# Kernel tuning notes

Measured on AMD Instinct MI355X. Metric: run time of the kernel, lower is better.

## Reference

```python
import jax, jax.numpy as jnp
import numpy as np

N_NODES = 50000
N_EDGES = 400000
IN_DIM = 8
HIDDEN = 768
N_LAYERS = 4
LN_EPS = 1e-5


def setup_inputs() -> dict:
    key = jax.random.key(0)
    ks = jax.random.split(key, 10)
    x = jax.random.normal(ks[0], (N_NODES, IN_DIM), dtype=jnp.float32)
    edge_index = jax.random.randint(ks[1], (2, N_EDGES), 0, N_NODES, dtype=jnp.int32)
    # input projection
    s_in = 1.0 / np.sqrt(IN_DIM)
    Wp = jax.random.uniform(ks[2], (HIDDEN, IN_DIM), jnp.float32, -s_in, s_in)
    bp = jax.random.uniform(ks[3], (HIDDEN,), jnp.float32, -s_in, s_in)
    # stacked per-layer SAGEConv params (all layers have out_c == HIDDEN here)
    s_h = 1.0 / np.sqrt(HIDDEN)
    Wl = jax.random.uniform(ks[4], (N_LAYERS, HIDDEN, HIDDEN), jnp.float32, -s_h, s_h)  # lin_l (aggregated neighbors), has bias
    bl = jax.random.uniform(ks[5], (N_LAYERS, HIDDEN), jnp.float32, -s_h, s_h)
    Wr = jax.random.uniform(ks[6], (N_LAYERS, HIDDEN, HIDDEN), jnp.float32, -s_h, s_h)  # lin_r (root), no bias
    # LayerNorm params
    gamma = jnp.ones((N_LAYERS, HIDDEN), dtype=jnp.float32)
    beta = jnp.zeros((N_LAYERS, HIDDEN), dtype=jnp.float32)
    return {"x": x, "Wp": Wp, "bp": bp, "Wl": Wl, "bl": bl, "Wr": Wr,
            "gamma": gamma, "beta": beta, "edge_index": edge_index}


def _layer_norm(h, g, b):
    mu = jnp.mean(h, axis=-1, keepdims=True)
    var = jnp.mean(jnp.square(h - mu), axis=-1, keepdims=True)
    return (h - mu) * jax.lax.rsqrt(var + LN_EPS) * g + b


def reference(x, Wp, bp, Wl, bl, Wr, gamma, beta, edge_index):
    n = x.shape[0]
    src, dst = edge_index[0], edge_index[1]
    # in-degree per target node, clamped for mean
    deg = jax.ops.segment_sum(jnp.ones_like(dst, dtype=x.dtype), dst, num_segments=n)
    inv_deg = 1.0 / jnp.maximum(deg, 1.0)

    h = x @ Wp.T + bp  # [N, HIDDEN]

    def layer(h, params):
        Wl_i, bl_i, Wr_i, g_i, b_i = params
        # mean aggregation of source features at targets: [N, C]
        agg = jax.ops.segment_sum(h[src], dst, num_segments=n) * inv_deg[:, None]
        out = agg @ Wl_i.T + bl_i + h @ Wr_i.T  # SAGEConv
        out = _layer_norm(jax.nn.silu(out), g_i, b_i)  # norm(silu(conv))
        return out, None

    h, _ = jax.lax.scan(layer, h, (Wl, bl, Wr, gamma, beta))
    return h
```

## Files before the change

### kernel.cpp

```cpp
#include <hip/hip_runtime.h>

#define NN 50000
#define NE 400000
#define HID 768
#define NL 4

typedef short bf16x8_t __attribute__((ext_vector_type(8)));
typedef float f32x4_t __attribute__((ext_vector_type(4)));

__device__ __forceinline__ unsigned short f2bf(float f) {
  union { float f; unsigned int u; } c; c.f = f;
  unsigned int u = c.u;
  u += 0x7FFF + ((u >> 16) & 1);
  return (unsigned short)(u >> 16);
}
__device__ __forceinline__ float bf2f(unsigned short s) {
  union { unsigned int u; float f; } c; c.u = ((unsigned int)s) << 16;
  return c.f;
}

__device__ __forceinline__ void async16(const void* g, void* l) {
  __builtin_amdgcn_global_load_lds((const __attribute__((address_space(1))) void*)g,
                                   (__attribute__((address_space(3))) void*)l,
                                   16, 0, 0);
}

__global__ void k_zero2(int* __restrict__ a, int* __restrict__ b, int n) {
  int i = blockIdx.x * blockDim.x + threadIdx.x;
  if (i < n) { a[i] = 0; b[i] = 0; }
}

__global__ void k_cvt(const float* __restrict__ a, unsigned short* __restrict__ o, int n) {
  int i = blockIdx.x * blockDim.x + threadIdx.x;
  if (i < n) o[i] = f2bf(a[i]);
}

__global__ __launch_bounds__(256) void k_inproj(const float* __restrict__ x,
                                                const float* __restrict__ Wp,
                                                const float* __restrict__ bp,
                                                unsigned short* __restrict__ h) {
  int n = blockIdx.x;
  __shared__ float xs[8];
  if (threadIdx.x < 8) xs[threadIdx.x] = x[n * 8 + threadIdx.x];
  __syncthreads();
  for (int j = threadIdx.x; j < HID; j += 256) {
    const float* w = Wp + j * 8;
    float s = bp[j];
#pragma unroll
    for (int k = 0; k < 8; ++k) s += xs[k] * w[k];
    h[(size_t)n * HID + j] = f2bf(s);
  }
}

__global__ void k_deg(const int* __restrict__ dst, int* __restrict__ deg) {
  int i = blockIdx.x * blockDim.x + threadIdx.x;
  if (i < NE) atomicAdd(&deg[dst[i]], 1);
}

__global__ __launch_bounds__(1024) void k_scan(const int* __restrict__ deg, int* __restrict__ rowptr) {
  __shared__ int sm[1024];
  const int chunk = 49;
  int t = threadIdx.x;
  int start = t * chunk;
  int end = min(start + chunk, NN);
  int local = 0;
  for (int i = start; i < end; ++i) local += deg[i];
  sm[t] = local;
  __syncthreads();
  for (int off = 1; off < 1024; off <<= 1) {
    int v = (t >= off) ? sm[t - off] : 0;
    __syncthreads();
    sm[t] += v;
    __syncthreads();
  }
  int run = sm[t] - local;
  for (int i = start; i < end; ++i) { rowptr[i] = run; run += deg[i]; }
  if (start < NN && end == NN) rowptr[NN] = run;
}

__global__ void k_fill(const int* __restrict__ src, const int* __restrict__ dst,
                       const int* __restrict__ rowptr, int* __restrict__ cursor,
                       int* __restrict__ csr) {
  int i = blockIdx.x * blockDim.x + threadIdx.x;
  if (i < NE) {
    int d = dst[i];
    int pos = atomicAdd(&cursor[d], 1);
    csr[rowptr[d] + pos] = src[i];
  }
}

__global__ __launch_bounds__(192) void k_agg(const unsigned short* __restrict__ h,
                                             const int* __restrict__ csr,
                                             const int* __restrict__ rowptr,
                                             unsigned short* __restrict__ agg) {
  int n = blockIdx.x;
  int t = threadIdx.x;
  int beg = rowptr[n], end = rowptr[n + 1];
  float a0 = 0.f, a1 = 0.f, a2 = 0.f, a3 = 0.f;
  for (int i = beg; i < end; ++i) {
    int s = csr[i];
    ushort4 v = *(const ushort4*)(h + (size_t)s * HID + t * 4);
    a0 += bf2f(v.x); a1 += bf2f(v.y); a2 += bf2f(v.z); a3 += bf2f(v.w);
  }
  float inv = 1.0f / (float)max(end - beg, 1);
  ushort4 o;
  o.x = f2bf(a0 * inv); o.y = f2bf(a1 * inv); o.z = f2bf(a2 * inv); o.w = f2bf(a3 * inv);
  *(ushort4*)(agg + (size_t)n * HID + t * 4) = o;
}

#define BM 224
#define BN 256
#define BKT 32
#define NKT 48
#define NBANDS 224

__global__ __launch_bounds__(512, 2) void k_gemm(const unsigned short* __restrict__ A0,
                                                 const unsigned short* __restrict__ A1,
                                                 const unsigned short* __restrict__ B0,
                                                 const unsigned short* __restrict__ B1,
                                                 const float* __restrict__ bias,
                                                 unsigned short* __restrict__ sact, int M) {
  __shared__ __align__(16) unsigned short As[2][256 * BKT];
  __shared__ __align__(16) unsigned short Bs[2][256 * BKT];

  int b = blockIdx.x;
  int xcd = b & 7;
  int rest = b >> 3;
  int nt3 = rest % 3;
  int g = rest / 3;
  int mband = g * 8 + xcd;
  int m0 = mband * BM;
  int n0 = nt3 * BN;

  int tid = threadIdx.x;
  int lane = tid & 63;
  int w = tid >> 6;
  int wm = w >> 2, wn = w & 3;

  int srow = w * 16 + (lane >> 2);
  int kgg = (lane & 3) ^ ((srow >> 1) & 3);
  size_t aoffg = (size_t)(m0 + srow) * HID + kgg * 8;
  size_t boffg = (size_t)(n0 + srow) * HID + kgg * 8;
  const size_t rstep = (size_t)128 * HID;

  auto stage = [&](int kt, int slot) {
    const unsigned short* A = (kt < 24) ? A0 : A1;
    const unsigned short* B = (kt < 24) ? B0 : B1;
    size_t kk = (size_t)((kt < 24) ? kt : kt - 24) * BKT;
    async16(A + aoffg + kk,         &As[slot][(w * 16) * BKT]);
    async16(B + boffg + kk,         &Bs[slot][(w * 16) * BKT]);
    async16(A + aoffg + rstep + kk, &As[slot][(128 + w * 16) * BKT]);
    async16(B + boffg + rstep + kk, &Bs[slot][(128 + w * 16) * BKT]);
  };

  int mr = lane & 15, kq = lane >> 4;
  int aoff[7], boff[4];
#pragma unroll
  for (int t = 0; t < 7; ++t) {
    int row = wm * 112 + t * 16 + mr;
    aoff[t] = row * BKT + ((kq ^ ((row >> 1) & 3)) * 8);
  }
#pragma unroll
  for (int t = 0; t < 4; ++t) {
    int row = wn * 64 + t * 16 + mr;
    boff[t] = row * BKT + ((kq ^ ((row >> 1) & 3)) * 8);
  }

  f32x4_t acc[7][4] = {};

  stage(0, 0);
  stage(1, 1);

#pragma unroll 2
  for (int T = 0; T < NKT; ++T) {
    int slot = T & 1;
    if (T < NKT - 1) asm volatile("s_waitcnt vmcnt(4)" ::: "memory");
    else             asm volatile("s_waitcnt vmcnt(0)" ::: "memory");
    __builtin_amdgcn_s_barrier();
    asm volatile("" ::: "memory");

    bf16x8_t af[7], bf[4];
#pragma unroll
    for (int t = 0; t < 7; ++t) af[t] = *(const bf16x8_t*)&As[slot][aoff[t]];
#pragma unroll
    for (int t = 0; t < 4; ++t) bf[t] = *(const bf16x8_t*)&Bs[slot][boff[t]];

    __builtin_amdgcn_s_setprio(1);
#pragma unroll
    for (int mt = 0; mt < 7; ++mt)
#pragma unroll
      for (int nt = 0; nt < 4; ++nt)
        acc[mt][nt] = __builtin_amdgcn_mfma_f32_16x16x32_bf16(af[mt], bf[nt], acc[mt][nt], 0, 0, 0);
    __builtin_amdgcn_s_setprio(0);

    asm volatile("s_waitcnt lgkmcnt(0)" ::: "memory");
    __builtin_amdgcn_s_barrier();
    if (T + 2 < NKT) stage(T + 2, slot);
  }

  int col = lane & 15;
  int rq = (lane >> 4) * 4;
#pragma unroll
  for (int mt = 0; mt < 7; ++mt) {
#pragma unroll
    for (int nt = 0; nt < 4; ++nt) {
      int j = n0 + wn * 64 + nt * 16 + col;
      float bv = bias[j];
#pragma unroll
      for (int r = 0; r < 4; ++r) {
        int gm = m0 + wm * 112 + mt * 16 + rq + r;
        if (gm < M) {
          float v = acc[mt][nt][r] + bv;
          float s = v / (1.f + __expf(-v));
          sact[(size_t)gm * HID + j] = f2bf(s);
        }
      }
    }
  }
}

__global__ __launch_bounds__(256) void k_ln(const unsigned short* __restrict__ sact,
                                            const float* __restrict__ gamma,
                                            const float* __restrict__ beta,
                                            unsigned short* __restrict__ hout,
                                            float* __restrict__ fout) {
  int n = blockIdx.x;
  const unsigned short* p = sact + (size_t)n * HID;
  float v[3];
  float sum = 0.f, sq = 0.f;
#pragma unroll
  for (int i = 0; i < 3; ++i) {
    float s = bf2f(p[threadIdx.x + i * 256]);
    v[i] = s; sum += s; sq += s * s;
  }
#pragma unroll
  for (int off = 32; off >= 1; off >>= 1) {
    sum += __shfl_down(sum, off);
    sq  += __shfl_down(sq, off);
  }
  __shared__ float rs[4], rq2[4];
  int wv = threadIdx.x >> 6;
  if ((threadIdx.x & 63) == 0) { rs[wv] = sum; rq2[wv] = sq; }
  __syncthreads();
  if (threadIdx.x == 0) {
    float s = rs[0] + rs[1] + rs[2] + rs[3];
    float q = rq2[0] + rq2[1] + rq2[2] + rq2[3];
    rs[0] = s / (float)HID;
    rq2[0] = q / (float)HID;
  }
  __syncthreads();
  float mu = rs[0];
  float var = rq2[0] - mu * mu;
  float inv = rsqrtf(var + 1e-5f);
#pragma unroll
  for (int i = 0; i < 3; ++i) {
    int j = threadIdx.x + i * 256;
    float y = (v[i] - mu) * inv * gamma[j] + beta[j];
    if (fout) fout[(size_t)n * HID + j] = y;
    else      hout[(size_t)n * HID + j] = f2bf(y);
  }
}

extern "C" void kernel_launch(void* const* d_in, const int* in_sizes, int n_in,
                              void* d_out, int out_size, void* d_ws, size_t ws_size,
                              hipStream_t stream) {
  const float* x     = (const float*)d_in[0];
  const float* Wp    = (const float*)d_in[1];
  const float* bp    = (const float*)d_in[2];
  const float* Wl    = (const float*)d_in[3];
  const float* bl    = (const float*)d_in[4];
  const float* Wr    = (const float*)d_in[5];
  const float* gamma = (const float*)d_in[6];
  const float* beta  = (const float*)d_in[7];
  const int*   ei    = (const int*)d_in[8];
  float* out = (float*)d_out;

  const int* src = ei;
  const int* dst = ei + NE;

  char* p = (char*)d_ws;
  unsigned short* h    = (unsigned short*)p;              p += (size_t)NN * HID * 2;
  unsigned short* agg  = (unsigned short*)p;              p += (size_t)NN * HID * 2;
  unsigned short* sact = (unsigned short*)p;              p += (size_t)NN * HID * 2;
  unsigned short* Wlb  = (unsigned short*)p;              p += (size_t)NL * HID * HID * 2;
  unsigned short* Wrb  = (unsigned short*)p;              p += (size_t)NL * HID * HID * 2;
  int* deg             = (int*)p;                         p += (size_t)NN * 4;
  int* rowptr          = (int*)p;                         p += (size_t)(NN + 1) * 4 + 12;
  int* cursor          = (int*)p;                         p += (size_t)NN * 4;
  int* csr             = (int*)p;                         p += (size_t)NE * 4;

  k_zero2<<<(NN + 255) / 256, 256, 0, stream>>>(deg, cursor, NN);
  int wn = NL * HID * HID;
  k_cvt<<<(wn + 255) / 256, 256, 0, stream>>>(Wl, Wlb, wn);
  k_cvt<<<(wn + 255) / 256, 256, 0, stream>>>(Wr, Wrb, wn);
  k_inproj<<<NN, 256, 0, stream>>>(x, Wp, bp, h);
  k_deg<<<(NE + 255) / 256, 256, 0, stream>>>(dst, deg);
  k_scan<<<1, 1024, 0, stream>>>(deg, rowptr);
  k_fill<<<(NE + 255) / 256, 256, 0, stream>>>(src, dst, rowptr, cursor, csr);

  const int ggrid = 8 * 3 * 28;
  for (int l = 0; l < NL; ++l) {
    k_agg<<<NN, 192, 0, stream>>>(h, csr, rowptr, agg);
    k_gemm<<<ggrid, 512, 0, stream>>>(agg, h,
                                      Wlb + (size_t)l * HID * HID,
                                      Wrb + (size_t)l * HID * HID,
                                      bl + (size_t)l * HID, sact, NN);
    k_ln<<<NN, 256, 0, stream>>>(sact, gamma + (size_t)l * HID, beta + (size_t)l * HID,
                                 h, (l == NL - 1) ? out : nullptr);
  }
}
```

Measured before the change: 1.673 ms.

## Enlarge GEMM tile to 256x256 with 4-stage split A/B prefetch pipeline

```diff
diff --git a/kernel.cpp b/kernel.cpp
--- a/kernel.cpp
+++ b/kernel.cpp
@@ -108,11 +108,10 @@
   *(ushort4*)(agg + (size_t)n * HID + t * 4) = o;
 }
 
-#define BM 224
+#define BM 256
 #define BN 256
-#define BKT 32
 #define NKT 48
-#define NBANDS 224
+#define GGRID 588
 
 __global__ __launch_bounds__(512, 2) void k_gemm(const unsigned short* __restrict__ A0,
                                                  const unsigned short* __restrict__ A1,
@@ -120,16 +119,16 @@
                                                  const unsigned short* __restrict__ B1,
                                                  const float* __restrict__ bias,
                                                  unsigned short* __restrict__ sact, int M) {
-  __shared__ __align__(16) unsigned short As[2][256 * BKT];
-  __shared__ __align__(16) unsigned short Bs[2][256 * BKT];
+  __shared__ __align__(16) unsigned short As[4][BM * 32];
+  __shared__ __align__(16) unsigned short Bs[4][BN * 32];
 
   int b = blockIdx.x;
   int xcd = b & 7;
-  int rest = b >> 3;
-  int nt3 = rest % 3;
-  int g = rest / 3;
-  int mband = g * 8 + xcd;
-  int m0 = mband * BM;
+  int j = b >> 3;
+  int o = xcd * 73 + min(xcd, 4) + j;
+  int band = o / 3;
+  int nt3 = o - band * 3;
+  int m0 = band * BM;
   int n0 = nt3 * BN;
 
   int tid = threadIdx.x;
@@ -137,82 +136,92 @@
   int w = tid >> 6;
   int wm = w >> 2, wn = w & 3;
 
-  int srow = w * 16 + (lane >> 2);
-  int kgg = (lane & 3) ^ ((srow >> 1) & 3);
-  size_t aoffg = (size_t)(m0 + srow) * HID + kgg * 8;
-  size_t boffg = (size_t)(n0 + srow) * HID + kgg * 8;
-  const size_t rstep = (size_t)128 * HID;
-
-  auto stage = [&](int kt, int slot) {
-    const unsigned short* A = (kt < 24) ? A0 : A1;
-    const unsigned short* B = (kt < 24) ? B0 : B1;
-    size_t kk = (size_t)((kt < 24) ? kt : kt - 24) * BKT;
-    async16(A + aoffg + kk,         &As[slot][(w * 16) * BKT]);
-    async16(B + boffg + kk,         &Bs[slot][(w * 16) * BKT]);
-    async16(A + aoffg + rstep + kk, &As[slot][(128 + w * 16) * BKT]);
-    async16(B + boffg + rstep + kk, &Bs[slot][(128 + w * 16) * BKT]);
+  int rl = tid >> 2;
+  int kgs = (tid & 3) ^ ((rl >> 1) & 3);
+  size_t aO = (size_t)(m0 + rl) * HID + kgs * 8;
+  size_t bO = (size_t)(n0 + rl) * HID + kgs * 8;
+  const size_t hstep = (size_t)128 * HID;
+
+  auto stageA = [&](int t) {
+    const unsigned short* A = (t < 24) ? A0 : A1;
+    size_t kk = (size_t)(t - ((t < 24) ? 0 : 24)) * 32;
+    int s = t & 3;
+    async16(A + aO + kk,         &As[s][w * 512]);
+    async16(A + aO + hstep + kk, &As[s][4096 + w * 512]);
   };
+  auto stageB = [&](int t) {
+    const unsigned short* B = (t < 24) ? B0 : B1;
+    size_t kk = (size_t)(t - ((t < 24) ? 0 : 24)) * 32;
+    int s = t & 3;
+    async16(B + bO + kk,         &Bs[s][w * 512]);
+    async16(B + bO + hstep + kk, &Bs[s][4096 + w * 512]);
+  };
 
   int mr = lane & 15, kq = lane >> 4;
-  int aoff[7], boff[4];
-#pragma unroll
-  for (int t = 0; t < 7; ++t) {
-    int row = wm * 112 + t * 16 + mr;
-    aoff[t] = row * BKT + ((kq ^ ((row >> 1) & 3)) * 8);
-  }
-#pragma unroll
-  for (int t = 0; t < 4; ++t) {
-    int row = wn * 64 + t * 16 + mr;
-    boff[t] = row * BKT + ((kq ^ ((row >> 1) & 3)) * 8);
-  }
-
-  f32x4_t acc[7][4] = {};
-
-  stage(0, 0);
-  stage(1, 1);
-
-#pragma unroll 2
-  for (int T = 0; T < NKT; ++T) {
-    int slot = T & 1;
-    if (T < NKT - 1) asm volatile("s_waitcnt vmcnt(4)" ::: "memory");
-    else             asm volatile("s_waitcnt vmcnt(0)" ::: "memory");
+  int sq = (kq ^ ((mr >> 1) & 3)) * 8;
+
+  f32x4_t acc[8][4] = {};
+
+  stageA(0); stageB(0); stageA(1); stageB(1); stageA(2);
+  asm volatile("s_waitcnt vmcnt(6)" ::: "memory");
+  __builtin_amdgcn_s_barrier();
+
+  for (int t = 0; t < NKT; ++t) {
+    int s = t & 3;
+    bf16x8_t af[4], ag[4], bf[4];
+#pragma unroll
+    for (int i = 0; i < 4; ++i)
+      af[i] = *(const bf16x8_t*)&As[s][(wm * 128 + i * 16 + mr) * 32 + sq];
+#pragma unroll
+    for (int i = 0; i < 4; ++i)
+      bf[i] = *(const bf16x8_t*)&Bs[s][(wn * 64 + i * 16 + mr) * 32 + sq];
+    if (t <= 45) stageB(t + 2);
     __builtin_amdgcn_s_barrier();
-    asm volatile("" ::: "memory");
-
-    bf16x8_t af[7], bf[4];
-#pragma unroll
-    for (int t = 0; t < 7; ++t) af[t] = *(const bf16x8_t*)&As[slot][aoff[t]];
-#pragma unroll
-    for (int t = 0; t < 4; ++t) bf[t] = *(const bf16x8_t*)&Bs[slot][boff[t]];
-
+    asm volatile("s_waitcnt lgkmcnt(0)" ::: "memory");
+    __builtin_amdgcn_sched_barrier(0);
     __builtin_amdgcn_s_setprio(1);
 #pragma unroll
-    for (int mt = 0; mt < 7; ++mt)
+    for (int mt = 0; mt < 4; ++mt)
 #pragma unroll
       for (int nt = 0; nt < 4; ++nt)
         acc[mt][nt] = __builtin_amdgcn_mfma_f32_16x16x32_bf16(af[mt], bf[nt], acc[mt][nt], 0, 0, 0);
     __builtin_amdgcn_s_setprio(0);
-
+    __builtin_amdgcn_s_barrier();
+#pragma unroll
+    for (int i = 0; i < 4; ++i)
+      ag[i] = *(const bf16x8_t*)&As[s][(wm * 128 + (i + 4) * 16 + mr) * 32 + sq];
+    if (t <= 44) stageA(t + 3);
+    __builtin_amdgcn_s_barrier();
     asm volatile("s_waitcnt lgkmcnt(0)" ::: "memory");
+    __builtin_amdgcn_sched_barrier(0);
+    __builtin_amdgcn_s_setprio(1);
+#pragma unroll
+    for (int mt = 0; mt < 4; ++mt)
+#pragma unroll
+      for (int nt = 0; nt < 4; ++nt)
+        acc[mt + 4][nt] = __builtin_amdgcn_mfma_f32_16x16x32_bf16(ag[mt], bf[nt], acc[mt + 4][nt], 0, 0, 0);
+    __builtin_amdgcn_s_setprio(0);
+    if (t <= 44)      asm volatile("s_waitcnt vmcnt(6)" ::: "memory");
+    else if (t == 45) asm volatile("s_waitcnt vmcnt(4)" ::: "memory");
+    else if (t == 46) asm volatile("s_waitcnt vmcnt(0)" ::: "memory");
     __builtin_amdgcn_s_barrier();
-    if (T + 2 < NKT) stage(T + 2, slot);
   }
 
   int col = lane & 15;
   int rq = (lane >> 4) * 4;
 #pragma unroll
-  for (int mt = 0; mt < 7; ++mt) {
+  for (int mt = 0; mt < 8; ++mt) {
 #pragma unroll
     for (int nt = 0; nt < 4; ++nt) {
-      int j = n0 + wn * 64 + nt * 16 + col;
-      float bv = bias[j];
+      int jj = n0 + wn * 64 + nt * 16 + col;
+      float bv = bias[jj];
 #pragma unroll
       for (int r = 0; r < 4; ++r) {
-        int gm = m0 + wm * 112 + mt * 16 + rq + r;
+        int gm = m0 + wm * 128 + mt * 16 + rq + r;
         if (gm < M) {
           float v = acc[mt][nt][r] + bv;
-          float s = v / (1.f + __expf(-v));
-          sact[(size_t)gm * HID + j] = f2bf(s);
+          float sv = v / (1.f + __expf(-v));
+          sact[(size_t)gm * HID + jj] = f2bf(sv);
         }
       }
     }
@@ -298,10 +307,9 @@
   k_scan<<<1, 1024, 0, stream>>>(deg, rowptr);
   k_fill<<<(NE + 255) / 256, 256, 0, stream>>>(src, dst, rowptr, cursor, csr);
 
-  const int ggrid = 8 * 3 * 28;
   for (int l = 0; l < NL; ++l) {
     k_agg<<<NN, 192, 0, stream>>>(h, csr, rowptr, agg);
-    k_gemm<<<ggrid, 512, 0, stream>>>(agg, h,
+    k_gemm<<<GGRID, 512, 0, stream>>>(agg, h,
                                       Wlb + (size_t)l * HID * HID,
                                       Wrb + (size_t)l * HID * HID,
                                       bl + (size_t)l * HID, sact, NN);
```

After: 1.742 ms. +4.1%, slower.
